# Performance work log

Hardware: AMD Instinct MI355X
Metric: run time of the kernel (lower is better)

The kernel has to match this reference:

```python
import jax, jax.numpy as jnp
import numpy as np

NEG = -1e9

def setup_inputs() -> dict:
    key = jax.random.key(0)
    k1, k2, k3, k4, k5, k6 = jax.random.split(key, 6)
    B, S, H = 8, 2048, 1024
    inputs = jax.random.normal(k1, (B, S, H), dtype=jnp.float32)
    mask = jax.random.randint(k2, (B, S, S), 0, 2) > 0  # bool [B,S,S]
    scale = 1.0 / np.sqrt(H)
    Wq = jax.random.normal(k3, (H, H), dtype=jnp.float32) * scale
    Wk = jax.random.normal(k4, (H, H), dtype=jnp.float32) * scale
    Wv = jax.random.normal(k5, (H, H), dtype=jnp.float32) * scale
    return {"inputs": inputs, "mask": mask, "Wq": Wq, "Wk": Wk, "Wv": Wv}

def reference(inputs, mask, Wq, Wk, Wv):
    H = inputs.shape[-1]
    # nn.Linear(x) = x @ W.T (bias=False)
    Q = jnp.einsum('bsh,dh->bsd', inputs, Wq)
    K = jnp.einsum('bsh,dh->bsd', inputs, Wk)
    V = jnp.einsum('bsh,dh->bsd', inputs, Wv)
    alpha = jnp.einsum('bqd,bkd->bqk', Q, K) / jnp.sqrt(jnp.float32(H))
    alpha = jnp.where(mask, NEG, alpha)
    alpha = jax.nn.softmax(alpha, axis=-1)
    return jnp.einsum('bqk,bkd->bqd', alpha, V)
```

## Files before the change

### kernel.cpp

```cpp
#include <hip/hip_runtime.h>
#include <hip/hip_bf16.h>
#include <hip/hip_fp16.h>
#include <stdint.h>

typedef __attribute__((ext_vector_type(4))) float    f32x4;
typedef __attribute__((ext_vector_type(8))) _Float16 f16x8;
typedef __attribute__((ext_vector_type(4))) _Float16 f16x4;

__device__ __forceinline__ f32x4 mfma16(f16x8 a, f16x8 b, f32x4 c) {
  return __builtin_amdgcn_mfma_f32_16x16x32_f16(a, b, c, 0, 0, 0);
}

__device__ __forceinline__ void store4(float* p, f32x4 v) { *(f32x4*)p = v; }
__device__ __forceinline__ void store4(_Float16* p, f32x4 v) {
  f16x4 h; h[0] = (_Float16)v[0]; h[1] = (_Float16)v[1];
  h[2] = (_Float16)v[2]; h[3] = (_Float16)v[3];
  *(f16x4*)p = h;
}

__device__ __forceinline__ void gload16(const _Float16* g, char* l) {
  __builtin_amdgcn_global_load_lds(
      (const __attribute__((address_space(1))) void*)g,
      (__attribute__((address_space(3))) void*)l, 16, 0, 0);
}

__device__ __forceinline__ bool src_is_f32(const void* p) {
  const unsigned* w = (const unsigned*)p;
  int sane = 0;
#pragma unroll
  for (int i = 0; i < 64; ++i) {
    const unsigned e = (w[i] >> 7) & 0xFFu;
    sane += (e >= 100u && e <= 140u) ? 1 : 0;
  }
  return sane < 40;
}

__device__ __forceinline__ float bf16_to_f32(unsigned u16) {
  union { unsigned u; float f; } c; c.u = u16 << 16; return c.f;
}

__device__ __forceinline__ f16x8 cvt8(const void* in, long i, bool f32) {
  f16x8 o;
  if (f32) {
    const float4 a = ((const float4*)in)[2 * i];
    const float4 b = ((const float4*)in)[2 * i + 1];
    o[0] = (_Float16)a.x; o[1] = (_Float16)a.y; o[2] = (_Float16)a.z; o[3] = (_Float16)a.w;
    o[4] = (_Float16)b.x; o[5] = (_Float16)b.y; o[6] = (_Float16)b.z; o[7] = (_Float16)b.w;
  } else {
    const uint4 v = ((const uint4*)in)[i];
    const unsigned wd[4] = {v.x, v.y, v.z, v.w};
#pragma unroll
    for (int j = 0; j < 4; ++j) {
      o[2 * j]     = (_Float16)bf16_to_f32(wd[j] & 0xFFFFu);
      o[2 * j + 1] = (_Float16)bf16_to_f32(wd[j] >> 16);
    }
  }
  return o;
}

__global__ __launch_bounds__(256)
void cvt_any_f16(const void* __restrict__ in, _Float16* __restrict__ out, long n8)
{
  const long i = (long)blockIdx.x * 256 + threadIdx.x;
  if (i >= n8) return;
  ((f16x8*)out)[i] = cvt8(in, i, src_is_f32(in));
}

__global__ __launch_bounds__(256)
void cvt_w3_f16(const void* __restrict__ w0, const void* __restrict__ w1,
                const void* __restrict__ w2, _Float16* __restrict__ out, long n8each)
{
  const long i = (long)blockIdx.x * 256 + threadIdx.x;
  if (i >= 3 * n8each) return;
  const int which = (int)(i / n8each);
  const long li = i - (long)which * n8each;
  const void* src = which == 0 ? w0 : (which == 1 ? w1 : w2);
  ((f16x8*)out)[i] = cvt8(src, li, src_is_f32(src));
}

__global__ __launch_bounds__(256)
void zerofill(float* out, long n) {
  const long i = (long)blockIdx.x * 256 + threadIdx.x;
  if (i < n) out[i] = 0.0f;
}

template <typename TO>
__global__ __launch_bounds__(512, 2)
void gemm256(const _Float16* __restrict__ Ag, const _Float16* __restrict__ Bg,
             TO* __restrict__ Cg, int ldA, int ldB, int ldC, int Kd,
             long sAb, long sBb, long sCb, float scale, int gx, int gy)
{
  extern __shared__ char smem[];

  const int nwg = gridDim.x;
  const int q = nwg >> 3, r = nwg & 7;
  const int xcd = blockIdx.x & 7, sub = blockIdx.x >> 3;
  const int wg = (xcd < r ? xcd * (q + 1) : r * (q + 1) + (xcd - r) * q) + sub;
  const int bz  = wg / (gx * gy);
  const int rem = wg % (gx * gy);
  const int by  = rem / gx;
  const int bx  = rem % gx;

  const _Float16* A = Ag + (long)bz * sAb + (long)by * 256 * ldA;
  const _Float16* B = Bg + (long)bz * sBb + (long)bx * 256 * ldB;
  TO* C = Cg + (long)bz * sCb;

  const int t   = threadIdx.x;
  const int ln  = t & 63;
  const int wid = t >> 6;
  const int wr  = wid >> 2;
  const int wc  = wid & 3;
  const int fr  = ln & 15;
  const int c16 = ln >> 4;

  const int sr = t >> 3;
  const int sc = t & 7;
  const int swzc = (sc ^ (sr & 7)) << 3;

  auto STAGE = [&](const _Float16* M, int ld, int matOff, int row0, int kt1) {
    const _Float16* src = M + (long)(row0 + sr) * ld + (kt1 << 6) + swzc;
    char* dst = smem + ((kt1 & 1) << 16) + matOff + (row0 << 7) + (t << 4);
    gload16(src, dst);
  };

  f32x4 acc[8][4] = {};

  STAGE(B, ldB, 32768,   0, 0);  STAGE(B, ldB, 32768,  64, 0);
  STAGE(B, ldB, 32768, 128, 0);  STAGE(B, ldB, 32768, 192, 0);
  STAGE(A, ldA,     0,   0, 0);  STAGE(A, ldA,     0, 128, 0);
  STAGE(A, ldA,     0,  64, 0);  STAGE(A, ldA,     0, 192, 0);
  asm volatile("s_waitcnt vmcnt(2)" ::: "memory");
  __builtin_amdgcn_s_barrier();

  const int NT = Kd >> 6;
  for (int kt = 0; kt < NT; ++kt) {
    const int bufOff = (kt & 1) << 16;
    const bool more = (kt + 1) < NT;

    auto LDA = [&](int mi, int kk) -> f16x8 {
      const int row = (wr << 7) + (mi << 4) + fr;
      const int ch  = ((kk << 2) + c16) ^ (row & 7);
      return *(const f16x8*)(smem + bufOff + (row << 7) + (ch << 4));
    };
    auto LDB = [&](int ni, int kk) -> f16x8 {
      const int row = (wc << 6) + (ni << 4) + fr;
      const int ch  = ((kk << 2) + c16) ^ (row & 7);
      return *(const f16x8*)(smem + bufOff + 32768 + (row << 7) + (ch << 4));
    };

    f16x8 bF[4][2];
#pragma unroll
    for (int p = 0; p < 4; ++p) {
      if (p == 0) {
#pragma unroll
        for (int ni = 0; ni < 4; ++ni)
#pragma unroll
          for (int kk = 0; kk < 2; ++kk) bF[ni][kk] = LDB(ni, kk);
      }
      f16x8 aF[2][2];
#pragma unroll
      for (int i = 0; i < 2; ++i)
#pragma unroll
        for (int kk = 0; kk < 2; ++kk) aF[i][kk] = LDA(2 * p + i, kk);

      if (more) {
        if (p == 0) { STAGE(B, ldB, 32768,   0, kt + 1); STAGE(B, ldB, 32768,  64, kt + 1); }
        if (p == 1) { STAGE(B, ldB, 32768, 128, kt + 1); STAGE(B, ldB, 32768, 192, kt + 1); }
        if (p == 2) { STAGE(A, ldA,     0,   0, kt + 1); STAGE(A, ldA,     0, 128, kt + 1); }
        if (p == 3) { STAGE(A, ldA,     0,  64, kt + 1); STAGE(A, ldA,     0, 192, kt + 1); }
      }

      __builtin_amdgcn_s_barrier();
      __builtin_amdgcn_s_setprio(1);
#pragma unroll
      for (int i = 0; i < 2; ++i)
#pragma unroll
        for (int ni = 0; ni < 4; ++ni)
#pragma unroll
          for (int kk = 0; kk < 2; ++kk)
            acc[2 * p + i][ni] = mfma16(aF[i][kk], bF[ni][kk], acc[2 * p + i][ni]);
      __builtin_amdgcn_s_setprio(0);

      if (p == 1) asm volatile("s_waitcnt vmcnt(4)" ::: "memory");
      if (p == 3) asm volatile("s_waitcnt vmcnt(2)" ::: "memory");
      __builtin_amdgcn_s_barrier();
    }
  }

  {
    char* wb = smem + wid * 4352;
    const int rr = (ln >> 4) << 2;
    const int rrow = ln >> 4;
    const int rch  = ln & 15;
#pragma unroll
    for (int mi = 0; mi < 8; ++mi) {
#pragma unroll
      for (int ni = 0; ni < 4; ++ni)
#pragma unroll
        for (int rq = 0; rq < 4; ++rq)
          *(float*)(wb + (((rr + rq) * 68) + (ni << 4) + fr) * 4) =
              scale * acc[mi][ni][rq];
#pragma unroll
      for (int it = 0; it < 4; ++it) {
        const int rloc = it * 4 + rrow;
        f32x4 v = *(const f32x4*)(wb + (rloc * 68 + rch * 4) * 4);
        const int row = by * 256 + wr * 128 + mi * 16 + rloc;
        const int col = bx * 256 + wc * 64 + rch * 4;
        store4(&C[(long)row * ldC + col], v);
      }
    }
  }
}

enum { MK_I32, MK_I64, MK_U16, MK_F32, MK_F64, MK_U8 };

__global__ __launch_bounds__(256)
void softmax_mask(_Float16* __restrict__ P, const void* __restrict__ maskp,
                  int S, long row0)
{
  const long lrow = blockIdx.x;
  const long grow = row0 + lrow;
  const int  t    = threadIdx.x;
  const int  w    = t >> 6;
  const int  ln   = t & 63;

  const unsigned* mw = (const unsigned*)maskp;
  bool le1 = true, u16p = true, f32p = true, f64p = true, oddz = true;
#pragma unroll
  for (int i = 0; i < 64; ++i) {
    const unsigned v = mw[i];
    if (v > 1u) le1 = false;
    if (v != 0u && v != 1u && v != 0x10000u && v != 0x10001u) u16p = false;
    if (v != 0u && v != 0x3F800000u) f32p = false;
    if (i & 1) { if (v != 0u && v != 0x3FF00000u) f64p = false; if (v) oddz = false; }
    else       { if (v > 1u) f64p = false; }
  }
  int mode;
  if (le1)        mode = oddz ? MK_I64 : MK_I32;
  else if (u16p)  mode = MK_U16;
  else if (f32p)  mode = MK_F32;
  else if (f64p)  mode = MK_F64;
  else            mode = MK_U8;

  _Float16* prow = P + lrow * S;
  f16x8 hv = *(const f16x8*)(prow + t * 8);

  const long mbase = grow * (long)S + t * 8;
  int mk[8];
  if (mode == MK_I32) {
    const int4* mp = (const int4*)((const int*)maskp + mbase);
    int4 a = mp[0], b = mp[1];
    mk[0] = a.x; mk[1] = a.y; mk[2] = a.z; mk[3] = a.w;
    mk[4] = b.x; mk[5] = b.y; mk[6] = b.z; mk[7] = b.w;
  } else if (mode == MK_U8) {
    const unsigned long long v = *(const unsigned long long*)((const unsigned char*)maskp + mbase);
#pragma unroll
    for (int j = 0; j < 8; ++j) mk[j] = (int)((v >> (8 * j)) & 0xffull);
  } else if (mode == MK_F32) {
    const uint4* mp = (const uint4*)((const unsigned*)maskp + mbase);
    uint4 a = mp[0], b = mp[1];
    mk[0] = a.x != 0; mk[1] = a.y != 0; mk[2] = a.z != 0; mk[3] = a.w != 0;
    mk[4] = b.x != 0; mk[5] = b.y != 0; mk[6] = b.z != 0; mk[7] = b.w != 0;
  } else if (mode == MK_I64 || mode == MK_F64) {
    const unsigned long long* mp = (const unsigned long long*)maskp + mbase;
#pragma unroll
    for (int j = 0; j < 8; ++j) mk[j] = mp[j] != 0ull;
  } else {
    const unsigned short* mp = (const unsigned short*)maskp + mbase;
#pragma unroll
    for (int j = 0; j < 8; ++j) mk[j] = mp[j] != 0;
  }

  float s[8];
#pragma unroll
  for (int j = 0; j < 8; ++j) s[j] = mk[j] ? -1e9f : (float)hv[j];

  float m = -3.0e38f;
#pragma unroll
  for (int j = 0; j < 8; ++j) m = fmaxf(m, s[j]);
#pragma unroll
  for (int d = 1; d < 64; d <<= 1) m = fmaxf(m, __shfl_xor(m, d));

  __shared__ float redm[4], reds[4];
  if (ln == 0) redm[w] = m;
  __syncthreads();
  m = fmaxf(fmaxf(redm[0], redm[1]), fmaxf(redm[2], redm[3]));

  float p[8], sum = 0.f;
#pragma unroll
  for (int j = 0; j < 8; ++j) { p[j] = __expf(s[j] - m); sum += p[j]; }
#pragma unroll
  for (int d = 1; d < 64; d <<= 1) sum += __shfl_xor(sum, d);
  if (ln == 0) reds[w] = sum;
  __syncthreads();
  sum = reds[0] + reds[1] + reds[2] + reds[3];
  const float inv = 1.0f / sum;

  f16x8 ov;
#pragma unroll
  for (int j = 0; j < 8; ++j) ov[j] = (_Float16)(p[j] * inv);
  *(f16x8*)(prow + t * 8) = ov;
}

extern "C" void kernel_launch(void* const* d_in, const int* in_sizes, int n_in,
                              void* d_out, int out_size, void* d_ws, size_t ws_size,
                              hipStream_t stream)
{
  const int B = 8, S = 2048, H = 1024;
  const long nXl = (long)B * S * H;
  const long nMl = (long)B * S * S;
  const long nWl = (long)H * H;

  const void* X = nullptr;
  const void* Mk = nullptr;
  const void* W[3] = {nullptr, nullptr, nullptr};
  int wi = 0;
  for (int i = 0; i < n_in; ++i) {
    const long sz = in_sizes[i];
    if (sz == nXl) X = d_in[i];
    else if (sz == nMl) Mk = d_in[i];
    else if (sz == nWl && wi < 3) W[wi++] = d_in[i];
  }
  float* Out = (float*)d_out;

  const size_t nX = (size_t)nXl, nW = (size_t)nWl;
  const size_t need2 = (4 * nX + 3 * nW) * 2;
  const size_t needP = (size_t)nMl * 2;
  const size_t need1 = need2 + needP;

  if (!X || !Mk || wi < 3 || ws_size < need2) {
    zerofill<<<dim3((unsigned)((out_size + 255) / 256)), dim3(256), 0, stream>>>(
        Out, (long)out_size);
    return;
  }
  const bool single = (ws_size >= need1);

  _Float16* Wh  = (_Float16*)d_ws;
  _Float16* QK2 = Wh  + 3 * nW;
  _Float16* Vt  = QK2 + 2 * nX;
  _Float16* Xh  = Vt  + nX;
  _Float16* P   = single ? (Xh + nX) : Xh;

  dim3 blk(256), gblk(512);
  const size_t GLDS = 131072;
  const long SH = (long)S * H, SS = (long)S * S, HS = (long)H * S;

  cvt_any_f16<<<dim3((unsigned)(nX / 8 / 256)), blk, 0, stream>>>(X, Xh, nX / 8);
  cvt_w3_f16<<<dim3((unsigned)(3 * nW / 8 / 256)), blk, 0, stream>>>(
      W[0], W[1], W[2], Wh, nW / 8);

  gemm256<_Float16><<<dim3(8 * 64), gblk, GLDS, stream>>>(
      Xh, Wh, QK2, H, H, 2 * H, H, 0L, 0L, 0L, 1.0f, 8, 64);
  gemm256<_Float16><<<dim3(8 * 4 * 8), gblk, GLDS, stream>>>(
      Wh + 2 * nW, Xh, Vt, H, H, S, H, 0L, SH, HS, 1.0f, 8, 4);

  const _Float16* Qp = QK2;
  const _Float16* Kp = QK2 + H;

  if (single) {
    gemm256<_Float16><<<dim3(8 * 8 * 8), gblk, GLDS, stream>>>(
        Qp, Kp, P, 2 * H, 2 * H, S, H, 2 * SH, 2 * SH, SS, 0.03125f, 8, 8);
    softmax_mask<<<dim3(B * S), blk, 0, stream>>>(P, Mk, S, 0L);
    gemm256<float><<<dim3(4 * 8 * 8), gblk, GLDS, stream>>>(
        P, Vt, Out, S, S, H, S, SS, HS, SH, 1.0f, 4, 8);
  } else {
    for (int g = 0; g < 2; ++g) {
      const int b0 = 4 * g;
      gemm256<_Float16><<<dim3(8 * 8 * 4), gblk, GLDS, stream>>>(
          Qp + (long)b0 * 2 * SH, Kp + (long)b0 * 2 * SH, P,
          2 * H, 2 * H, S, H, 2 * SH, 2 * SH, SS, 0.03125f, 8, 8);
      softmax_mask<<<dim3(4 * S), blk, 0, stream>>>(P, Mk, S, (long)b0 * S);
      gemm256<float><<<dim3(4 * 8 * 4), gblk, GLDS, stream>>>(
          P, Vt + (long)b0 * HS, Out + (long)b0 * SH,
          S, S, H, S, SS, HS, SH, 1.0f, 4, 8);
    }
  }
}
```

Before: 366.5 us.

## Classify mask once and use one wave per softmax row

Result: faster. 318.2 us (-13.2%).

```diff
diff --git a/kernel.cpp b/kernel.cpp
--- a/kernel.cpp
+++ b/kernel.cpp
@@ -84,6 +84,30 @@
   if (i < n) out[i] = 0.0f;
 }
 
+enum { MK_I32, MK_I64, MK_U16, MK_F32, MK_F64, MK_U8 };
+
+__global__ void classify_mask(const void* __restrict__ maskp, int* __restrict__ out)
+{
+  if (threadIdx.x != 0 || blockIdx.x != 0) return;
+  const unsigned* mw = (const unsigned*)maskp;
+  bool le1 = true, u16p = true, f32p = true, f64p = true, oddz = true;
+  for (int i = 0; i < 64; ++i) {
+    const unsigned v = mw[i];
+    if (v > 1u) le1 = false;
+    if (v != 0u && v != 1u && v != 0x10000u && v != 0x10001u) u16p = false;
+    if (v != 0u && v != 0x3F800000u) f32p = false;
+    if (i & 1) { if (v != 0u && v != 0x3FF00000u) f64p = false; if (v) oddz = false; }
+    else       { if (v > 1u) f64p = false; }
+  }
+  int mode;
+  if (le1)        mode = oddz ? MK_I64 : MK_I32;
+  else if (u16p)  mode = MK_U16;
+  else if (f32p)  mode = MK_F32;
+  else if (f64p)  mode = MK_F64;
+  else            mode = MK_U8;
+  *out = mode;
+}
+
 template <typename TO>
 __global__ __launch_bounds__(512, 2)
 void gemm256(const _Float16* __restrict__ Ag, const _Float16* __restrict__ Bg,
@@ -212,94 +236,97 @@
   }
 }
 
-enum { MK_I32, MK_I64, MK_U16, MK_F32, MK_F64, MK_U8 };
-
 __global__ __launch_bounds__(256)
-void softmax_mask(_Float16* __restrict__ P, const void* __restrict__ maskp,
-                  int S, long row0)
-{
-  const long lrow = blockIdx.x;
+void softmax_wave(_Float16* __restrict__ P, const void* __restrict__ maskp,
+                  const int* __restrict__ modep, int S, long row0)
+{
+  const int  mode = *modep;
+  const long lrow = (long)blockIdx.x * 4 + (threadIdx.x >> 6);
   const long grow = row0 + lrow;
-  const int  t    = threadIdx.x;
-  const int  w    = t >> 6;
-  const int  ln   = t & 63;
-
-  const unsigned* mw = (const unsigned*)maskp;
-  bool le1 = true, u16p = true, f32p = true, f64p = true, oddz = true;
-#pragma unroll
-  for (int i = 0; i < 64; ++i) {
-    const unsigned v = mw[i];
-    if (v > 1u) le1 = false;
-    if (v != 0u && v != 1u && v != 0x10000u && v != 0x10001u) u16p = false;
-    if (v != 0u && v != 0x3F800000u) f32p = false;
-    if (i & 1) { if (v != 0u && v != 0x3FF00000u) f64p = false; if (v) oddz = false; }
-    else       { if (v > 1u) f64p = false; }
-  }
-  int mode;
-  if (le1)        mode = oddz ? MK_I64 : MK_I32;
-  else if (u16p)  mode = MK_U16;
-  else if (f32p)  mode = MK_F32;
-  else if (f64p)  mode = MK_F64;
-  else            mode = MK_U8;
+  const int  ln   = threadIdx.x & 63;
 
   _Float16* prow = P + lrow * S;
-  f16x8 hv = *(const f16x8*)(prow + t * 8);
-
-  const long mbase = grow * (long)S + t * 8;
-  int mk[8];
-  if (mode == MK_I32) {
-    const int4* mp = (const int4*)((const int*)maskp + mbase);
-    int4 a = mp[0], b = mp[1];
-    mk[0] = a.x; mk[1] = a.y; mk[2] = a.z; mk[3] = a.w;
-    mk[4] = b.x; mk[5] = b.y; mk[6] = b.z; mk[7] = b.w;
-  } else if (mode == MK_U8) {
-    const unsigned long long v = *(const unsigned long long*)((const unsigned char*)maskp + mbase);
-#pragma unroll
-    for (int j = 0; j < 8; ++j) mk[j] = (int)((v >> (8 * j)) & 0xffull);
+  f16x8 pv[4];
+#pragma unroll
+  for (int j = 0; j < 4; ++j)
+    pv[j] = *(const f16x8*)(prow + j * 512 + ln * 8);
+
+  const long ebase = grow * (long)S;
+  int mk[4][8];
+  if (mode == MK_U8) {
+    const unsigned char* m = (const unsigned char*)maskp + ebase;
+#pragma unroll
+    for (int j = 0; j < 4; ++j) {
+      const unsigned long long v = *(const unsigned long long*)(m + j * 512 + ln * 8);
+#pragma unroll
+      for (int k = 0; k < 8; ++k) mk[j][k] = (int)((v >> (8 * k)) & 0xffull);
+    }
+  } else if (mode == MK_I32) {
+    const int* m = (const int*)maskp + ebase;
+#pragma unroll
+    for (int j = 0; j < 4; ++j) {
+      const int4 a = *(const int4*)(m + j * 512 + ln * 8);
+      const int4 b = *(const int4*)(m + j * 512 + ln * 8 + 4);
+      mk[j][0] = a.x; mk[j][1] = a.y; mk[j][2] = a.z; mk[j][3] = a.w;
+      mk[j][4] = b.x; mk[j][5] = b.y; mk[j][6] = b.z; mk[j][7] = b.w;
+    }
   } else if (mode == MK_F32) {
-    const uint4* mp = (const uint4*)((const unsigned*)maskp + mbase);
-    uint4 a = mp[0], b = mp[1];
-    mk[0] = a.x != 0; mk[1] = a.y != 0; mk[2] = a.z != 0; mk[3] = a.w != 0;
-    mk[4] = b.x != 0; mk[5] = b.y != 0; mk[6] = b.z != 0; mk[7] = b.w != 0;
-  } else if (mode == MK_I64 || mode == MK_F64) {
-    const unsigned long long* mp = (const unsigned long long*)maskp + mbase;
-#pragma unroll
-    for (int j = 0; j < 8; ++j) mk[j] = mp[j] != 0ull;
+    const unsigned* m = (const unsigned*)maskp + ebase;
+#pragma unroll
+    for (int j = 0; j < 4; ++j) {
+      const uint4 a = *(const uint4*)(m + j * 512 + ln * 8);
+      const uint4 b = *(const uint4*)(m + j * 512 + ln * 8 + 4);
+      mk[j][0] = a.x != 0; mk[j][1] = a.y != 0; mk[j][2] = a.z != 0; mk[j][3] = a.w != 0;
+      mk[j][4] = b.x != 0; mk[j][5] = b.y != 0; mk[j][6] = b.z != 0; mk[j][7] = b.w != 0;
+    }
+  } else if (mode == MK_U16) {
+    const unsigned short* m = (const unsigned short*)maskp + ebase;
+#pragma unroll
+    for (int j = 0; j < 4; ++j) {
+      const uint4 v = *(const uint4*)(m + j * 512 + ln * 8);
+      const unsigned wd[4] = {v.x, v.y, v.z, v.w};
+#pragma unroll
+      for (int k = 0; k < 4; ++k) {
+        mk[j][2 * k]     = (wd[k] & 0xFFFFu) != 0;
+        mk[j][2 * k + 1] = (wd[k] >> 16) != 0;
+      }
+    }
   } else {
-    const unsigned short* mp = (const unsigned short*)maskp + mbase;
-#pragma unroll
-    for (int j = 0; j < 8; ++j) mk[j] = mp[j] != 0;
-  }
-
-  float s[8];
-#pragma unroll
-  for (int j = 0; j < 8; ++j) s[j] = mk[j] ? -1e9f : (float)hv[j];
-
-  float m = -3.0e38f;
-#pragma unroll
-  for (int j = 0; j < 8; ++j) m = fmaxf(m, s[j]);
-#pragma unroll
-  for (int d = 1; d < 64; d <<= 1) m = fmaxf(m, __shfl_xor(m, d));
-
-  __shared__ float redm[4], reds[4];
-  if (ln == 0) redm[w] = m;
-  __syncthreads();
-  m = fmaxf(fmaxf(redm[0], redm[1]), fmaxf(redm[2], redm[3]));
-
-  float p[8], sum = 0.f;
-#pragma unroll
-  for (int j = 0; j < 8; ++j) { p[j] = __expf(s[j] - m); sum += p[j]; }
+    const unsigned long long* m = (const unsigned long long*)maskp + ebase;
+#pragma unroll
+    for (int j = 0; j < 4; ++j)
+#pragma unroll
+      for (int k = 0; k < 8; ++k) mk[j][k] = m[j * 512 + ln * 8 + k] != 0ull;
+  }
+
+  float s[4][8];
+  float mx = -3.0e38f;
+#pragma unroll
+  for (int j = 0; j < 4; ++j)
+#pragma unroll
+    for (int k = 0; k < 8; ++k) {
+      s[j][k] = mk[j][k] ? -1e9f : (float)pv[j][k];
+      mx = fmaxf(mx, s[j][k]);
+    }
+#pragma unroll
+  for (int d = 1; d < 64; d <<= 1) mx = fmaxf(mx, __shfl_xor(mx, d));
+
+  float sum = 0.f;
+#pragma unroll
+  for (int j = 0; j < 4; ++j)
+#pragma unroll
+    for (int k = 0; k < 8; ++k) { s[j][k] = __expf(s[j][k] - mx); sum += s[j][k]; }
 #pragma unroll
   for (int d = 1; d < 64; d <<= 1) sum += __shfl_xor(sum, d);
-  if (ln == 0) reds[w] = sum;
-  __syncthreads();
-  sum = reds[0] + reds[1] + reds[2] + reds[3];
   const float inv = 1.0f / sum;
 
-  f16x8 ov;
-#pragma unroll
-  for (int j = 0; j < 8; ++j) ov[j] = (_Float16)(p[j] * inv);
-  *(f16x8*)(prow + t * 8) = ov;
+#pragma unroll
+  for (int j = 0; j < 4; ++j) {
+    f16x8 ov;
+#pragma unroll
+    for (int k = 0; k < 8; ++k) ov[k] = (_Float16)(s[j][k] * inv);
+    *(f16x8*)(prow + j * 512 + ln * 8) = ov;
+  }
 }
 
 extern "C" void kernel_launch(void* const* d_in, const int* in_sizes, int n_in,
@@ -328,23 +355,25 @@
   const size_t needP = (size_t)nMl * 2;
   const size_t need1 = need2 + needP;
 
-  if (!X || !Mk || wi < 3 || ws_size < need2) {
+  if (!X || !Mk || wi < 3 || ws_size < need2 + 256) {
     zerofill<<<dim3((unsigned)((out_size + 255) / 256)), dim3(256), 0, stream>>>(
         Out, (long)out_size);
     return;
   }
-  const bool single = (ws_size >= need1);
+  const bool single = (ws_size >= need1 + 256);
 
   _Float16* Wh  = (_Float16*)d_ws;
   _Float16* QK2 = Wh  + 3 * nW;
   _Float16* Vt  = QK2 + 2 * nX;
   _Float16* Xh  = Vt  + nX;
   _Float16* P   = single ? (Xh + nX) : Xh;
+  int* modeSlot = (int*)((char*)d_ws + (single ? need1 : need2));
 
   dim3 blk(256), gblk(512);
   const size_t GLDS = 131072;
   const long SH = (long)S * H, SS = (long)S * S, HS = (long)H * S;
 
+  classify_mask<<<dim3(1), dim3(64), 0, stream>>>(Mk, modeSlot);
   cvt_any_f16<<<dim3((unsigned)(nX / 8 / 256)), blk, 0, stream>>>(X, Xh, nX / 8);
   cvt_w3_f16<<<dim3((unsigned)(3 * nW / 8 / 256)), blk, 0, stream>>>(
       W[0], W[1], W[2], Wh, nW / 8);
@@ -360,7 +389,7 @@
   if (single) {
     gemm256<_Float16><<<dim3(8 * 8 * 8), gblk, GLDS, stream>>>(
         Qp, Kp, P, 2 * H, 2 * H, S, H, 2 * SH, 2 * SH, SS, 0.03125f, 8, 8);
-    softmax_mask<<<dim3(B * S), blk, 0, stream>>>(P, Mk, S, 0L);
+    softmax_wave<<<dim3(B * S / 4), blk, 0, stream>>>(P, Mk, modeSlot, S, 0L);
     gemm256<float><<<dim3(4 * 8 * 8), gblk, GLDS, stream>>>(
         P, Vt, Out, S, S, H, S, SS, HS, SH, 1.0f, 4, 8);
   } else {
@@ -369,7 +398,7 @@
       gemm256<_Float16><<<dim3(8 * 8 * 4), gblk, GLDS, stream>>>(
           Qp + (long)b0 * 2 * SH, Kp + (long)b0 * 2 * SH, P,
           2 * H, 2 * H, S, H, 2 * SH, 2 * SH, SS, 0.03125f, 8, 8);
-      softmax_mask<<<dim3(4 * S), blk, 0, stream>>>(P, Mk, S, (long)b0 * S);
+      softmax_wave<<<dim3(4 * S / 4), blk, 0, stream>>>(P, Mk, modeSlot, S, (long)b0 * S);
       gemm256<float><<<dim3(4 * 8 * 4), gblk, GLDS, stream>>>(
           P, Vt + (long)b0 * HS, Out + (long)b0 * SH,
           S, S, H, S, SS, HS, SH, 1.0f, 4, 8);
```
